# Kernel tuning notes

Measured on AMD Instinct MI355X. Metric: run time of the kernel, lower is better.

## Reference

```python
import jax, jax.numpy as jnp
import numpy as np

B, S, D, H = 2, 2048, 1024, 16
DK = D // H


def setup_inputs() -> dict:
    key = jax.random.key(0)
    ks = jax.random.split(key, 11)
    s = 1.0 / np.sqrt(D)
    inp = {
        "q": jax.random.normal(ks[0], (B, S, D), jnp.float32),
        "k": jax.random.normal(ks[1], (B, S, D), jnp.float32),
        "v": jax.random.normal(ks[2], (B, S, D), jnp.float32),
        "mask": jnp.tril(jnp.ones((S, S), jnp.int32))[None, None],  # [1,1,S,S] causal
        "Wq": jax.random.normal(ks[3], (D, D), jnp.float32) * s,
        "bq": jnp.zeros((D,), jnp.float32),
        "Wk": jax.random.normal(ks[4], (D, D), jnp.float32) * s,
        "bk": jnp.zeros((D,), jnp.float32),
        "Wv": jax.random.normal(ks[5], (D, D), jnp.float32) * s,
        "bv": jnp.zeros((D,), jnp.float32),
        "Wo": jax.random.normal(ks[6], (D, D), jnp.float32) * s,
        "bo": jnp.zeros((D,), jnp.float32),
    }
    return inp


def reference(q, k, v, mask, Wq, bq, Wk, bk, Wv, bv, Wo, bo):
    # projections -> [B, H, S, DK]
    def split_heads(x):
        return x.reshape(B, S, H, DK).transpose(0, 2, 1, 3)

    Q = split_heads(q @ Wq + bq)
    K = split_heads(k @ Wk + bk)
    V = split_heads(v @ Wv + bv)

    scores = jnp.einsum("bhqd,bhkd->bhqk", Q, K) / jnp.sqrt(jnp.float32(DK))
    scores = jnp.where(mask == 0, jnp.float32(-1e9), scores)
    # source applies dropout(p=0.0) here -> identity
    attn = jax.nn.softmax(scores, axis=-1)  # [B,H,S,S]
    x = jnp.einsum("bhqk,bhkd->bhqd", attn, V)
    x = x.transpose(0, 2, 1, 3).reshape(B, S, D)
    return x @ Wo + bo
```

## Files before the change

### kernel.cpp

```cpp
#include <hip/hip_runtime.h>
#include <hip/hip_bf16.h>
#include <stdint.h>

#define Bb 2
#define Ss 2048
#define Dd 1024
#define Hh 16
#define DKk 64

#define QSCALE 0.180336878f

typedef __attribute__((ext_vector_type(8))) short s8v;
typedef __attribute__((ext_vector_type(4))) short s4v;
typedef __attribute__((ext_vector_type(4))) float f4v;
typedef __attribute__((ext_vector_type(16))) float f16v;

#if __has_builtin(__builtin_amdgcn_exp2f)
#define EXP2(x) __builtin_amdgcn_exp2f(x)
#else
#define EXP2(x) __expf((x)*0.69314718f)
#endif

__device__ __forceinline__ unsigned short f2bf(float f) {
    __hip_bfloat16 h = __float2bfloat16(f);
    union { __hip_bfloat16 h; unsigned short u; } c; c.h = h;
    return c.u;
}

__device__ __forceinline__ unsigned pack_bf2(float lo, float hi) {
    __hip_bfloat162 h = __float22bfloat162_rn(float2{lo, hi});
    union { __hip_bfloat162 h; unsigned u; } c; c.h = h;
    return c.u;
}

__device__ __forceinline__ void gload16(const void* g, void* l) {
    __builtin_amdgcn_global_load_lds((__attribute__((address_space(1))) void*)g,
                                     (__attribute__((address_space(3))) void*)l, 16, 0, 0);
}

__global__ void __launch_bounds__(256) prep_x(const float* __restrict__ q,
                                              const float* __restrict__ k,
                                              const float* __restrict__ v,
                                              unsigned short* __restrict__ xq,
                                              unsigned short* __restrict__ xk,
                                              unsigned short* __restrict__ xv) {
    const int z = blockIdx.z;
    const float* s = (z == 0) ? q : ((z == 1) ? k : v);
    unsigned short* d = (z == 0) ? xq : ((z == 1) ? xk : xv);
    long i = ((long)blockIdx.x * blockDim.x + threadIdx.x) * 8;
    f4v a = *(const f4v*)(s + i);
    f4v b = *(const f4v*)(s + i + 4);
    union { unsigned u[4]; s8v v; } o;
    o.u[0] = pack_bf2(a[0], a[1]);
    o.u[1] = pack_bf2(a[2], a[3]);
    o.u[2] = pack_bf2(b[0], b[1]);
    o.u[3] = pack_bf2(b[2], b[3]);
    *(s8v*)(void*)(d + i) = o.v;
}

__global__ void __launch_bounds__(256) prep_w(const float* __restrict__ Wq,
                                              const float* __restrict__ Wk,
                                              const float* __restrict__ Wv,
                                              const float* __restrict__ Wo,
                                              unsigned short* __restrict__ o0,
                                              unsigned short* __restrict__ o1,
                                              unsigned short* __restrict__ o2,
                                              unsigned short* __restrict__ o3) {
    __shared__ float t[64][65];
    const int z = blockIdx.z;
    const float* W = (z == 0) ? Wq : ((z == 1) ? Wk : ((z == 2) ? Wv : Wo));
    unsigned short* O = (z == 0) ? o0 : ((z == 1) ? o1 : ((z == 2) ? o2 : o3));
    const int n0 = (blockIdx.x & 15) * 64;
    const int k0 = (blockIdx.x >> 4) * 64;
    const int c = threadIdx.x & 63;
    const int r4 = threadIdx.x >> 6;
#pragma unroll
    for (int i = 0; i < 16; i++) {
        int r = i * 4 + r4;
        t[r][c] = W[(long)(k0 + r) * Dd + n0 + c];
    }
    __syncthreads();
#pragma unroll
    for (int i = 0; i < 16; i++) {
        int r = i * 4 + r4;
        O[(long)(n0 + r) * Dd + k0 + c] = f2bf(t[c][r]);
    }
}

template <int MODE>
__device__ __forceinline__ void gemm_body(const unsigned short* __restrict__ A,
                                          const unsigned short* __restrict__ Bt,
                                          const float* __restrict__ bias,
                                          void* __restrict__ out, float oscale,
                                          unsigned short* smem, int m0, int n0) {
    unsigned short* As = smem;
    unsigned short* Bs = smem + 128 * 64;
    const int tid = threadIdx.x;
    const int l = tid & 63;
    const int w = tid >> 6;
    const int wr = w >> 1, wc = w & 1;
    const int lr = l & 15, lg = l >> 4;

    f4v acc[4][4];
#pragma unroll
    for (int m = 0; m < 4; m++)
#pragma unroll
        for (int n = 0; n < 4; n++) acc[m][n] = (f4v){0.f, 0.f, 0.f, 0.f};

    const int srow = tid >> 3;
    const int sg = (tid & 7) ^ (srow & 7);
    char* lbaseA = (char*)As + w * 1024;
    char* lbaseB = (char*)Bs + w * 1024;

#define STAGE_T(t_)                                                                    \
    do {                                                                               \
        const int k0_ = (t_) * 64;                                                     \
        _Pragma("unroll") for (int i_ = 0; i_ < 4; i_++) {                             \
            int rowA_ = i_ * 32 + srow;                                                \
            gload16((const char*)A + ((long)(m0 + rowA_) * 1024 + k0_) * 2 + sg * 16,  \
                    lbaseA + i_ * 4096);                                               \
            gload16((const char*)Bt + ((long)(n0 + rowA_) * 1024 + k0_) * 2 + sg * 16, \
                    lbaseB + i_ * 4096);                                               \
        }                                                                              \
    } while (0)

    STAGE_T(0);
    for (int t = 0; t < 16; t++) {
        asm volatile("s_waitcnt vmcnt(0)" ::: "memory");
        __builtin_amdgcn_s_barrier();
        __builtin_amdgcn_sched_barrier(0);

        s8v af[2][4], bfr[2][4];
#pragma unroll
        for (int kk = 0; kk < 2; kk++) {
#pragma unroll
            for (int m = 0; m < 4; m++) {
                int row = wr * 64 + m * 16 + lr;
                int gc = (kk * 4 + lg) ^ (row & 7);
                af[kk][m] = *(const s8v*)((const char*)As + row * 128 + gc * 16);
            }
#pragma unroll
            for (int n = 0; n < 4; n++) {
                int row = wc * 64 + n * 16 + lr;
                int gc = (kk * 4 + lg) ^ (row & 7);
                bfr[kk][n] = *(const s8v*)((const char*)Bs + row * 128 + gc * 16);
            }
        }
        asm volatile("s_waitcnt lgkmcnt(0)" ::: "memory");
        __builtin_amdgcn_sched_barrier(0);
        __builtin_amdgcn_s_barrier();
        __builtin_amdgcn_sched_barrier(0);

        if (t + 1 < 16) STAGE_T(t + 1);

#pragma unroll
        for (int kk = 0; kk < 2; kk++)
#pragma unroll
            for (int m = 0; m < 4; m++)
#pragma unroll
                for (int n = 0; n < 4; n++)
                    acc[m][n] = __builtin_amdgcn_mfma_f32_16x16x32_bf16(
                        af[kk][m], bfr[kk][n], acc[m][n], 0, 0, 0);
    }
#undef STAGE_T

#pragma unroll
    for (int n = 0; n < 4; n++) {
        int col = n0 + wc * 64 + n * 16 + lr;
        float bv = bias[col];
#pragma unroll
        for (int m = 0; m < 4; m++) {
#pragma unroll
            for (int r = 0; r < 4; r++) {
                int row = m0 + wr * 64 + m * 16 + lg * 4 + r;
                float val = acc[m][n][r] + bv;
                if (MODE == 0) {
                    int b = row >> 11, s2 = row & 2047, h = col >> 6, d = col & 63;
                    ((unsigned short*)out)[(((b * Hh + h) * Ss + s2) << 6) + d] =
                        f2bf(val * oscale);
                } else if (MODE == 1) {
                    int b = row >> 11, s2 = row & 2047, h = col >> 6, d = col & 63;
                    ((unsigned short*)out)[((b * Hh + h) * DKk + d) * Ss + s2] = f2bf(val);
                } else {
                    ((float*)out)[(long)row * Dd + col] = val;
                }
            }
        }
    }
}

__device__ __forceinline__ void xcd_tile(int bid, int& m0, int& n0) {
    int content = (bid & 7) * 32 + (bid >> 3);
    n0 = (content & 7) * 128;
    m0 = (content >> 3) * 128;
}

__global__ void __launch_bounds__(256) qkv_gemm(const unsigned short* __restrict__ xq,
                                                const unsigned short* __restrict__ xk,
                                                const unsigned short* __restrict__ xv,
                                                const unsigned short* __restrict__ Wqt,
                                                const unsigned short* __restrict__ Wkt,
                                                const unsigned short* __restrict__ Wvt,
                                                const float* __restrict__ bq,
                                                const float* __restrict__ bk,
                                                const float* __restrict__ bv,
                                                unsigned short* __restrict__ Qh,
                                                unsigned short* __restrict__ Kh,
                                                unsigned short* __restrict__ Vt) {
    __shared__ unsigned short smem[128 * 64 * 2];
    int m0, n0;
    xcd_tile(blockIdx.x, m0, n0);
    const int z = blockIdx.z;
    if (z == 0)
        gemm_body<0>(xq, Wqt, bq, Qh, QSCALE, smem, m0, n0);
    else if (z == 1)
        gemm_body<0>(xk, Wkt, bk, Kh, 1.f, smem, m0, n0);
    else
        gemm_body<1>(xv, Wvt, bv, Vt, 1.f, smem, m0, n0);
}

__global__ void __launch_bounds__(256) out_gemm(const unsigned short* __restrict__ x,
                                                const unsigned short* __restrict__ Wot,
                                                const float* __restrict__ bo,
                                                float* __restrict__ out) {
    __shared__ unsigned short smem[128 * 64 * 2];
    int m0, n0;
    xcd_tile(blockIdx.x, m0, n0);
    gemm_body<2>(x, Wot, bo, out, 1.f, smem, m0, n0);
}

__global__ void __launch_bounds__(256) attn_kernel(const unsigned short* __restrict__ Qh,
                                                   const unsigned short* __restrict__ Kh,
                                                   const unsigned short* __restrict__ Vt,
                                                   unsigned short* __restrict__ xatt) {
    __shared__ __align__(16) char ldsbuf[32768];
    unsigned short* Ks = (unsigned short*)ldsbuf;
    unsigned short* Vs = (unsigned short*)(ldsbuf + 16384);
    const int tid = threadIdx.x;
    const int w = tid >> 6, l = tid & 63;
    const int lq = l & 31;
    const int hi = l >> 5;
    const int bh = blockIdx.x & 31;
    const int tile = 63 - (blockIdx.x >> 5);
    const int q0 = tile * 32;
    const int b = bh >> 4, h = bh & 15;
    const unsigned short* Qp = Qh + bh * Ss * DKk;
    const unsigned short* Kp = Kh + bh * Ss * DKk;
    const unsigned short* Vp = Vt + bh * DKk * Ss;

    s8v qf[4];
#pragma unroll
    for (int kk = 0; kk < 4; kk++)
        qf[kk] = *(const s8v*)(Qp + (q0 + lq) * 64 + kk * 16 + hi * 8);

    f16v oT0, oT1;
#pragma unroll
    for (int r = 0; r < 16; r++) { oT0[r] = 0.f; oT1[r] = 0.f; }
    float mx = -1e30f, sm = 0.f;
    const int nkb = tile + 1;
    const int nch = (nkb + 3) >> 2;

    for (int ch = 0; ch < nch; ch++) {
        const int kv0 = ch * 128;
#pragma unroll
        for (int i = 0; i < 4; i++) {
            const int G0 = i * 256 + w * 64;
            int G = G0 + l;
            int row = G >> 3, gd = G & 7;
            int gs = gd ^ (row & 7);
            gload16(Kp + (kv0 + row) * 64 + gs * 8, (char*)Ks + G0 * 16);
        }
#pragma unroll
        for (int i = 0; i < 4; i++) {
            const int G0 = i * 256 + w * 64;
            int G = G0 + l;
            int row = G >> 4, gd = G & 15;
            int gs = gd ^ (row & 15);
            gload16(Vp + (long)row * Ss + kv0 + gs * 8, (char*)Vs + G0 * 16);
        }
        __syncthreads();

        const int kb = ch * 4 + w;
        if (kb < nkb) {
            const int k0 = kb * 32;
            s8v kf[4];
#pragma unroll
            for (int kk = 0; kk < 4; kk++) {
                int row = w * 32 + lq;
                int g = (2 * kk + hi) ^ (row & 7);
                kf[kk] = *(const s8v*)((const char*)Ks + (row * 8 + g) * 16);
            }
            s8v vf0[2], vf1[2];
#pragma unroll
            for (int kk = 0; kk < 2; kk++) {
                int g0 = 4 * w + 2 * kk + hi;
                vf0[kk] = *(const s8v*)((const char*)Vs + (lq * 16 + (g0 ^ (lq & 15))) * 16);
                vf1[kk] =
                    *(const s8v*)((const char*)Vs + ((32 + lq) * 16 + (g0 ^ (lq & 15))) * 16);
            }

            f16v S;
#pragma unroll
            for (int r = 0; r < 16; r++) S[r] = 0.f;
#pragma unroll
            for (int kk = 0; kk < 4; kk++)
                S = __builtin_amdgcn_mfma_f32_32x32x16_bf16(kf[kk], qf[kk], S, 0, 0, 0);

            const bool diag = (kb == nkb - 1);
            float e[16];
#pragma unroll
            for (int r = 0; r < 16; r++) {
                float v = S[r];
                if (diag) {
                    int kv = k0 + (r & 3) + 8 * (r >> 2) + 4 * hi;
                    if (kv > q0 + lq) v = -1e30f;
                }
                e[r] = v;
            }
            float m8[8];
#pragma unroll
            for (int i = 0; i < 8; i++) m8[i] = fmaxf(e[i], e[i + 8]);
#pragma unroll
            for (int i = 0; i < 4; i++) m8[i] = fmaxf(m8[i], m8[i + 4]);
            float pmax = fmaxf(fmaxf(m8[0], m8[1]), fmaxf(m8[2], m8[3]));
            pmax = fmaxf(pmax, __shfl_xor(pmax, 32));

            if (!__all(pmax - mx <= 8.f)) {
                float mn = fmaxf(mx, pmax);
                float sc = EXP2(mx - mn);
                mx = mn;
                sm *= sc;
#pragma unroll
                for (int r = 0; r < 16; r++) { oT0[r] *= sc; oT1[r] *= sc; }
            }
#pragma unroll
            for (int r = 0; r < 16; r++) e[r] = EXP2(e[r] - mx);
            float s8s[8];
#pragma unroll
            for (int i = 0; i < 8; i++) s8s[i] = e[i] + e[i + 8];
#pragma unroll
            for (int i = 0; i < 4; i++) s8s[i] = s8s[i] + s8s[i + 4];
            float rs = (s8s[0] + s8s[1]) + (s8s[2] + s8s[3]);
            sm += rs + __shfl_xor(rs, 32);

            unsigned pk[8], sw[8];
#pragma unroll
            for (int i = 0; i < 8; i++) pk[i] = pack_bf2(e[2 * i], e[2 * i + 1]);
#pragma unroll
            for (int i = 0; i < 8; i++) sw[i] = (unsigned)__shfl_xor((int)pk[i], 32);
            union { unsigned u[4]; s8v v; } p0, p1;
            p0.u[0] = hi ? sw[2] : pk[0];
            p0.u[1] = hi ? sw[3] : pk[1];
            p0.u[2] = hi ? pk[2] : sw[0];
            p0.u[3] = hi ? pk[3] : sw[1];
            p1.u[0] = hi ? sw[6] : pk[4];
            p1.u[1] = hi ? sw[7] : pk[5];
            p1.u[2] = hi ? pk[6] : sw[4];
            p1.u[3] = hi ? pk[7] : sw[5];

            oT0 = __builtin_amdgcn_mfma_f32_32x32x16_bf16(vf0[0], p0.v, oT0, 0, 0, 0);
            oT0 = __builtin_amdgcn_mfma_f32_32x32x16_bf16(vf0[1], p1.v, oT0, 0, 0, 0);
            oT1 = __builtin_amdgcn_mfma_f32_32x32x16_bf16(vf1[0], p0.v, oT1, 0, 0, 0);
            oT1 = __builtin_amdgcn_mfma_f32_32x32x16_bf16(vf1[1], p1.v, oT1, 0, 0, 0);
        }
        __syncthreads();
    }

    float(*plds)[64][34] = (float(*)[64][34])ldsbuf;
    if (w >= 2) {
        float* p = plds[w - 2][l];
        p[0] = mx; p[1] = sm;
#pragma unroll
        for (int r = 0; r < 16; r++) { p[2 + r] = oT0[r]; p[18 + r] = oT1[r]; }
    }
    __syncthreads();
    if (w < 2) {
        const float* p = plds[w][l];
        float m2 = p[0], s2 = p[1];
        float M = fmaxf(mx, m2);
        float a = EXP2(mx - M), bb = EXP2(m2 - M);
        sm = sm * a + s2 * bb;
#pragma unroll
        for (int r = 0; r < 16; r++) {
            oT0[r] = oT0[r] * a + p[2 + r] * bb;
            oT1[r] = oT1[r] * a + p[18 + r] * bb;
        }
        mx = M;
    }
    __syncthreads();
    if (w == 1) {
        float* p = plds[0][l];
        p[0] = mx; p[1] = sm;
#pragma unroll
        for (int r = 0; r < 16; r++) { p[2 + r] = oT0[r]; p[18 + r] = oT1[r]; }
    }
    __syncthreads();
    if (w != 0) return;
    {
        const float* p = plds[0][l];
        float m2 = p[0], s2 = p[1];
        float M = fmaxf(mx, m2);
        float a = EXP2(mx - M), bb = EXP2(m2 - M);
        sm = sm * a + s2 * bb;
#pragma unroll
        for (int r = 0; r < 16; r++) {
            oT0[r] = oT0[r] * a + p[2 + r] * bb;
            oT1[r] = oT1[r] * a + p[18 + r] * bb;
        }
    }

    const float inv = 1.f / sm;
    const int q = q0 + lq;
    unsigned short* orow = xatt + (long)(b * Ss + q) * Dd + h * 64;
#pragma unroll
    for (int g = 0; g < 4; g++) {
        union { unsigned u[2]; s4v v; } v0, v1;
        v0.u[0] = pack_bf2(oT0[g * 4 + 0] * inv, oT0[g * 4 + 1] * inv);
        v0.u[1] = pack_bf2(oT0[g * 4 + 2] * inv, oT0[g * 4 + 3] * inv);
        v1.u[0] = pack_bf2(oT1[g * 4 + 0] * inv, oT1[g * 4 + 1] * inv);
        v1.u[1] = pack_bf2(oT1[g * 4 + 2] * inv, oT1[g * 4 + 3] * inv);
        int d = 8 * g + 4 * hi;
        *(s4v*)(orow + d) = v0.v;
        *(s4v*)(orow + 32 + d) = v1.v;
    }
}

extern "C" void kernel_launch(void* const* d_in, const int* in_sizes, int n_in,
                              void* d_out, int out_size, void* d_ws, size_t ws_size,
                              hipStream_t stream) {
    const float* q  = (const float*)d_in[0];
    const float* k  = (const float*)d_in[1];
    const float* v  = (const float*)d_in[2];
    const float* Wq = (const float*)d_in[4];
    const float* bq = (const float*)d_in[5];
    const float* Wk = (const float*)d_in[6];
    const float* bk = (const float*)d_in[7];
    const float* Wv = (const float*)d_in[8];
    const float* bv = (const float*)d_in[9];
    const float* Wo = (const float*)d_in[10];
    const float* bo = (const float*)d_in[11];
    float* out = (float*)d_out;

    char* ws = (char*)d_ws;
    unsigned short* xq  = (unsigned short*)(ws + 0);
    unsigned short* xk  = (unsigned short*)(ws + 8388608);
    unsigned short* xv  = (unsigned short*)(ws + 16777216);
    unsigned short* Wqt = (unsigned short*)(ws + 25165824);
    unsigned short* Wkt = (unsigned short*)(ws + 27262976);
    unsigned short* Wvt = (unsigned short*)(ws + 29360128);
    unsigned short* Wot = (unsigned short*)(ws + 31457280);
    unsigned short* Qh  = (unsigned short*)(ws + 33554432);
    unsigned short* Kh  = (unsigned short*)(ws + 41943040);
    unsigned short* Vtp = (unsigned short*)(ws + 50331648);
    unsigned short* xat = (unsigned short*)(ws + 58720256);

    prep_x<<<dim3(2048, 1, 3), 256, 0, stream>>>(q, k, v, xq, xk, xv);
    prep_w<<<dim3(256, 1, 4), 256, 0, stream>>>(Wq, Wk, Wv, Wo, Wqt, Wkt, Wvt, Wot);
    qkv_gemm<<<dim3(256, 1, 3), 256, 0, stream>>>(xq, xk, xv, Wqt, Wkt, Wvt,
                                                  bq, bk, bv, Qh, Kh, Vtp);
    attn_kernel<<<dim3(2048), 256, 0, stream>>>(Qh, Kh, Vtp, xat);
    out_gemm<<<dim3(256), 256, 0, stream>>>(xat, Wot, bo, out);
}
```

Baseline: 134.3 us.

## Prefetch next K/V chunk into LDS while computing current chunk

New measurement: 133.4 us (median of 2 runs). Within noise of the previous version (-0.7%).

```diff
diff --git a/kernel.cpp b/kernel.cpp
--- a/kernel.cpp
+++ b/kernel.cpp
@@ -260,45 +260,55 @@
     const int nkb = tile + 1;
     const int nch = (nkb + 3) >> 2;
 
+#define STAGE_CH(ch_)                                                          \
+    do {                                                                       \
+        const int kv0_ = (ch_) * 128;                                          \
+        _Pragma("unroll") for (int i_ = 0; i_ < 4; i_++) {                     \
+            const int G0_ = i_ * 256 + w * 64;                                 \
+            int G_ = G0_ + l;                                                  \
+            int row_ = G_ >> 3, gd_ = G_ & 7;                                  \
+            int gs_ = gd_ ^ (row_ & 7);                                        \
+            gload16(Kp + (kv0_ + row_) * 64 + gs_ * 8, (char*)Ks + G0_ * 16);  \
+        }                                                                      \
+        _Pragma("unroll") for (int i_ = 0; i_ < 4; i_++) {                     \
+            const int G0_ = i_ * 256 + w * 64;                                 \
+            int G_ = G0_ + l;                                                  \
+            int row_ = G_ >> 4, gd_ = G_ & 15;                                 \
+            int gs_ = gd_ ^ (row_ & 15);                                       \
+            gload16(Vp + (long)row_ * Ss + kv0_ + gs_ * 8, (char*)Vs + G0_ * 16); \
+        }                                                                      \
+    } while (0)
+
+    STAGE_CH(0);
     for (int ch = 0; ch < nch; ch++) {
-        const int kv0 = ch * 128;
-#pragma unroll
-        for (int i = 0; i < 4; i++) {
-            const int G0 = i * 256 + w * 64;
-            int G = G0 + l;
-            int row = G >> 3, gd = G & 7;
-            int gs = gd ^ (row & 7);
-            gload16(Kp + (kv0 + row) * 64 + gs * 8, (char*)Ks + G0 * 16);
-        }
-#pragma unroll
-        for (int i = 0; i < 4; i++) {
-            const int G0 = i * 256 + w * 64;
-            int G = G0 + l;
-            int row = G >> 4, gd = G & 15;
-            int gs = gd ^ (row & 15);
-            gload16(Vp + (long)row * Ss + kv0 + gs * 8, (char*)Vs + G0 * 16);
-        }
-        __syncthreads();
+        asm volatile("s_waitcnt vmcnt(0)" ::: "memory");
+        __builtin_amdgcn_s_barrier();
+        __builtin_amdgcn_sched_barrier(0);
+
+        s8v kf[4], vf0[2], vf1[2];
+#pragma unroll
+        for (int kk = 0; kk < 4; kk++) {
+            int row = w * 32 + lq;
+            int g = (2 * kk + hi) ^ (row & 7);
+            kf[kk] = *(const s8v*)((const char*)Ks + (row * 8 + g) * 16);
+        }
+#pragma unroll
+        for (int kk = 0; kk < 2; kk++) {
+            int g0 = 4 * w + 2 * kk + hi;
+            vf0[kk] = *(const s8v*)((const char*)Vs + (lq * 16 + (g0 ^ (lq & 15))) * 16);
+            vf1[kk] =
+                *(const s8v*)((const char*)Vs + ((32 + lq) * 16 + (g0 ^ (lq & 15))) * 16);
+        }
+        asm volatile("s_waitcnt lgkmcnt(0)" ::: "memory");
+        __builtin_amdgcn_sched_barrier(0);
+        __builtin_amdgcn_s_barrier();
+        __builtin_amdgcn_sched_barrier(0);
+
+        if (ch + 1 < nch) STAGE_CH(ch + 1);
 
         const int kb = ch * 4 + w;
         if (kb < nkb) {
             const int k0 = kb * 32;
-            s8v kf[4];
-#pragma unroll
-            for (int kk = 0; kk < 4; kk++) {
-                int row = w * 32 + lq;
-                int g = (2 * kk + hi) ^ (row & 7);
-                kf[kk] = *(const s8v*)((const char*)Ks + (row * 8 + g) * 16);
-            }
-            s8v vf0[2], vf1[2];
-#pragma unroll
-            for (int kk = 0; kk < 2; kk++) {
-                int g0 = 4 * w + 2 * kk + hi;
-                vf0[kk] = *(const s8v*)((const char*)Vs + (lq * 16 + (g0 ^ (lq & 15))) * 16);
-                vf1[kk] =
-                    *(const s8v*)((const char*)Vs + ((32 + lq) * 16 + (g0 ^ (lq & 15))) * 16);
-            }
-
             f16v S;
 #pragma unroll
             for (int r = 0; r < 16; r++) S[r] = 0.f;
@@ -363,8 +373,8 @@
             oT1 = __builtin_amdgcn_mfma_f32_32x32x16_bf16(vf1[0], p0.v, oT1, 0, 0, 0);
             oT1 = __builtin_amdgcn_mfma_f32_32x32x16_bf16(vf1[1], p1.v, oT1, 0, 0, 0);
         }
-        __syncthreads();
-    }
+    }
+#undef STAGE_CH
 
     float(*plds)[64][34] = (float(*)[64][34])ldsbuf;
     if (w >= 2) {
```
